# Kernel tuning notes

Measured on AMD Instinct MI355X. Metric: run time of the kernel, lower is better.

The kernel has to match this reference:

```python
import jax, jax.numpy as jnp
import numpy as np

EMBED = 1024
HEADS = 16
HDIM = EMBED // HEADS
B, S = 4, 2048
NEG = -1e20


def setup_inputs() -> dict:
    key = jax.random.key(0)
    ks = jax.random.split(key, 9)
    query = jax.random.normal(ks[0], (B, S, EMBED), dtype=jnp.float32)
    key_t = jax.random.normal(ks[1], (B, S, EMBED), dtype=jnp.float32)
    value = jax.random.normal(ks[2], (B, S, EMBED), dtype=jnp.float32)
    mask = jax.random.randint(ks[3], (1, 1, S, S), 0, 2, dtype=jnp.int32)
    padding = jax.random.randint(ks[4], (B, 1, 1, S), 0, 2, dtype=jnp.int32)
    sc = 1.0 / np.sqrt(EMBED)
    Wq = jax.random.normal(ks[5], (EMBED, EMBED), dtype=jnp.float32) * sc
    Wk = jax.random.normal(ks[6], (EMBED, EMBED), dtype=jnp.float32) * sc
    Wv = jax.random.normal(ks[7], (EMBED, EMBED), dtype=jnp.float32) * sc
    Wo = jax.random.normal(ks[8], (EMBED, EMBED), dtype=jnp.float32) * sc
    return {"query": query, "key": key_t, "value": value, "mask": mask,
            "padding": padding, "Wq": Wq, "Wk": Wk, "Wv": Wv, "Wo": Wo}


def reference(query, key, value, mask, padding, Wq, Wk, Wv, Wo):
    b, q_len, _ = query.shape
    k_len = key.shape[1]
    # projections (nn.Linear: x @ W^T), split into heads
    qs = (query @ Wq.T).reshape(b, q_len, HEADS, HDIM)
    ks = (key @ Wk.T).reshape(b, k_len, HEADS, HDIM)
    vs = (value @ Wv.T).reshape(b, k_len, HEADS, HDIM)
    scale = EMBED ** 0.25
    qs = qs / scale
    ks = ks / scale
    # [b, h, q, k] scores
    dot = jnp.einsum('bkhd,bqhd->bhqk', ks, qs)
    dot = jnp.where(mask == 0, NEG, dot)
    dot = jnp.where(padding == 0, NEG, dot)
    attn = jax.nn.softmax(dot, axis=-1)
    alpha = jnp.einsum('bhqk,bkhd->bqhd', attn, vs)
    out = alpha.reshape(b, q_len, EMBED) @ Wo.T
    return out
```

## Files before the change

kernel.cpp:

```cpp
#include <hip/hip_runtime.h>
#include <stdint.h>

#define B_  4
#define S_  2048
#define E_  1024
#define H_  16
#define D_  64

typedef __bf16 bf16;
typedef __bf16 bf16x4 __attribute__((ext_vector_type(4)));
typedef __bf16 bf16x8 __attribute__((ext_vector_type(8)));
typedef float  f32x4 __attribute__((ext_vector_type(4)));
typedef float  f32x16 __attribute__((ext_vector_type(16)));
typedef uint32_t u32x4 __attribute__((ext_vector_type(4)));

__device__ __forceinline__ f32x4 mfma16(bf16x8 a, bf16x8 b, f32x4 c) {
  return __builtin_amdgcn_mfma_f32_16x16x32_bf16(a, b, c, 0, 0, 0);
}
__device__ __forceinline__ f32x16 mfma32(bf16x8 a, bf16x8 b, f32x16 c) {
  return __builtin_amdgcn_mfma_f32_32x32x16_bf16(a, b, c, 0, 0, 0);
}

__device__ __forceinline__ int sw(int row, int idx) { return idx ^ ((row & 7) << 3); }

__device__ __forceinline__ void gl_lds16(const void* g, void* l) {
  __builtin_amdgcn_global_load_lds(
      (const __attribute__((address_space(1))) void*)g,
      (__attribute__((address_space(3))) void*)l, 16, 0, 0);
}

__device__ __forceinline__ uint32_t cvtpk(float lo, float hi) {
  uint32_t r;
  asm("v_cvt_pk_bf16_f32 %0, %1, %2" : "=v"(r) : "v"(lo), "v"(hi));
  return r;
}
__device__ __forceinline__ void plswap(uint32_t& a, uint32_t& b) {
  asm("v_permlane32_swap_b32 %0, %1" : "+v"(a), "+v"(b));
}

__global__ void pack_mask_kernel(const int* __restrict__ mask, uint32_t* __restrict__ mbits) {
  int idx = blockIdx.x * 256 + threadIdx.x;
  int q = idx >> 6, w = idx & 63;
  const int* p = mask + q * S_ + w * 32;
  uint32_t bits = 0;
#pragma unroll
  for (int j = 0; j < 32; j += 4) {
    int4 v = *(const int4*)(p + j);
    bits |= (v.x != 0 ? 1u : 0u) << (j + 0);
    bits |= (v.y != 0 ? 1u : 0u) << (j + 1);
    bits |= (v.z != 0 ? 1u : 0u) << (j + 2);
    bits |= (v.w != 0 ? 1u : 0u) << (j + 3);
  }
  mbits[idx] = bits;
}

__global__ void pack_pad_kernel(const int* __restrict__ pad, uint32_t* __restrict__ pbits) {
  int idx = threadIdx.x;
  int b = idx >> 6, w = idx & 63;
  const int* p = pad + b * S_ + w * 32;
  uint32_t bits = 0;
#pragma unroll
  for (int j = 0; j < 32; j += 4) {
    int4 v = *(const int4*)(p + j);
    bits |= (v.x != 0 ? 1u : 0u) << (j + 0);
    bits |= (v.y != 0 ? 1u : 0u) << (j + 1);
    bits |= (v.z != 0 ? 1u : 0u) << (j + 2);
    bits |= (v.w != 0 ? 1u : 0u) << (j + 3);
  }
  pbits[idx] = bits;
}

__global__ __launch_bounds__(256)
void cvt_act(const float* __restrict__ q, const float* __restrict__ k,
             const float* __restrict__ v, bf16* __restrict__ out) {
  const float* src = blockIdx.z == 0 ? q : (blockIdx.z == 1 ? k : v);
  size_t i = ((size_t)blockIdx.x * 256 + threadIdx.x) * 8;
  float4 a = *(const float4*)(src + i);
  float4 b = *(const float4*)(src + i + 4);
  bf16x8 o;
  o[0] = (bf16)a.x; o[1] = (bf16)a.y; o[2] = (bf16)a.z; o[3] = (bf16)a.w;
  o[4] = (bf16)b.x; o[5] = (bf16)b.y; o[6] = (bf16)b.z; o[7] = (bf16)b.w;
  *(bf16x8*)(out + (size_t)blockIdx.z * (8192ull * 1024ull) + i) = o;
}

__global__ __launch_bounds__(256)
void cvt_w(const float* __restrict__ w0, const float* __restrict__ w1,
           const float* __restrict__ w2, const float* __restrict__ w3,
           bf16* __restrict__ out, float sq, float sk) {
  int z = blockIdx.z;
  const float* src = z == 0 ? w0 : (z == 1 ? w1 : (z == 2 ? w2 : w3));
  float s = (z == 0) ? sq : ((z == 1) ? sk : 1.0f);
  size_t i = ((size_t)blockIdx.x * 256 + threadIdx.x) * 8;
  float4 a = *(const float4*)(src + i);
  float4 b = *(const float4*)(src + i + 4);
  bf16x8 o;
  o[0] = (bf16)(a.x * s); o[1] = (bf16)(a.y * s); o[2] = (bf16)(a.z * s); o[3] = (bf16)(a.w * s);
  o[4] = (bf16)(b.x * s); o[5] = (bf16)(b.y * s); o[6] = (bf16)(b.z * s); o[7] = (bf16)(b.w * s);
  *(bf16x8*)(out + (size_t)z * (1024ull * 1024ull) + i) = o;
}

struct GA { const bf16* A; const bf16* W; void* O; };

template<bool OUT_F32>
__global__ __launch_bounds__(256, 2)
void gemm_bf(GA g0, GA g1, GA g2) {
  GA g = (blockIdx.z == 0) ? g0 : ((blockIdx.z == 1) ? g1 : g2);
  const int tid = threadIdx.x;
  const int l = tid & 63, wv = tid >> 6;
  const int lg = l >> 4, lr = l & 15;
  const int wr = wv >> 1, wc = wv & 1;
  const int brow = blockIdx.x * 128, bcol = blockIdx.y * 128;
  const int sr = l >> 3, sc8 = l & 7;

  __shared__ bf16 Ls[2][128 * 64];
  bf16* As = Ls[0];
  bf16* Bs = Ls[1];

  f32x4 acc[4][4] = {};

  const bf16* Ab = g.A + (size_t)(brow + wv * 32 + sr) * E_ + (size_t)(sc8 ^ sr) * 8;
  const bf16* Bb = g.W + (size_t)(bcol + wv * 32 + sr) * E_ + (size_t)(sc8 ^ sr) * 8;
  bf16* la = As + (wv * 32) * 64;
  bf16* lb = Bs + (wv * 32) * 64;

  for (int kt = 0; kt < E_ / 64; ++kt) {
    __syncthreads();
    const bf16* a = Ab + kt * 64;
    const bf16* b = Bb + kt * 64;
#pragma unroll
    for (int i = 0; i < 4; ++i) {
      gl_lds16(a + (size_t)i * 8 * E_, la + i * 8 * 64);
      gl_lds16(b + (size_t)i * 8 * E_, lb + i * 8 * 64);
    }
    __syncthreads();
#pragma unroll
    for (int kk = 0; kk < 2; ++kk) {
      bf16x8 af[4], bfr[4];
#pragma unroll
      for (int ms = 0; ms < 4; ++ms) {
        int row = wr * 64 + ms * 16 + lr;
        af[ms] = *(const bf16x8*)&As[sw(row, row * 64 + kk * 32 + lg * 8)];
      }
#pragma unroll
      for (int ns = 0; ns < 4; ++ns) {
        int row = wc * 64 + ns * 16 + lr;
        bfr[ns] = *(const bf16x8*)&Bs[sw(row, row * 64 + kk * 32 + lg * 8)];
      }
#pragma unroll
      for (int ms = 0; ms < 4; ++ms)
#pragma unroll
        for (int ns = 0; ns < 4; ++ns)
          acc[ms][ns] = mfma16(af[ms], bfr[ns], acc[ms][ns]);
    }
  }

  if (!OUT_F32 && blockIdx.z == 2) {
    bf16* T = &Ls[0][0];
    __syncthreads();
#pragma unroll
    for (int ms = 0; ms < 4; ++ms) {
#pragma unroll
      for (int ns = 0; ns < 4; ++ns) {
        int col = wc * 64 + ns * 16 + lr;
        int rowb = wr * 64 + ms * 16 + lg * 4;
        bf16x4 hv;
#pragma unroll
        for (int r = 0; r < 4; ++r) hv[r] = (bf16)acc[ms][ns][r];
        *(bf16x4*)&T[col * 128 + (rowb ^ ((col & 7) << 3))] = hv;
      }
    }
    __syncthreads();
    int chunk = tid & 15, dl0 = tid >> 4;
#pragma unroll
    for (int pass = 0; pass < 8; ++pass) {
      int dl = pass * 16 + dl0;
      bf16x8 v = *(const bf16x8*)&T[dl * 128 + ((chunk * 8) ^ ((dl & 7) << 3))];
      int colg = bcol + dl;
      int bh2 = (brow >> 11) * 16 + (colg >> 6);
      int d = colg & 63;
      int s0 = (brow & 2047) + chunk * 8;
      *(bf16x8*)((bf16*)g.O + ((size_t)bh2 * 64 + d) * (size_t)S_ + s0) = v;
    }
    return;
  }

#pragma unroll
  for (int ms = 0; ms < 4; ++ms) {
#pragma unroll
    for (int ns = 0; ns < 4; ++ns) {
#pragma unroll
      for (int r = 0; r < 4; ++r) {
        int row = brow + wr * 64 + ms * 16 + lg * 4 + r;
        int col = bcol + wc * 64 + ns * 16 + lr;
        if constexpr (OUT_F32) ((float*)g.O)[(size_t)row * E_ + col] = acc[ms][ns][r];
        else                   ((bf16*)g.O)[(size_t)row * E_ + col] = (bf16)acc[ms][ns][r];
      }
    }
  }
}

__global__ __launch_bounds__(256, 4)
void attn_kernel(const bf16* __restrict__ Q, const bf16* __restrict__ K,
                 const bf16* __restrict__ Vt, const uint32_t* __restrict__ mbits,
                 const uint32_t* __restrict__ pbits, bf16* __restrict__ alpha) {
  const int raw = blockIdx.x;
  const int xcd = raw & 7, slot = raw >> 3;
  const int bh = xcd * 8 + (slot >> 4), qblk = slot & 15;
  const int b = bh >> 4, h = bh & 15;
  const int tid = threadIdx.x, wv = tid >> 6, l = tid & 63;
  const int ln = l & 31, hi = l >> 5;
  const int qw = qblk * 128 + wv * 32;
  const int sr = l >> 3, sc8 = l & 7;
  const int g = (ln & 7) ^ (ln >> 3);

  __shared__ bf16 Ks[2][64 * 64];
  __shared__ bf16 Vs[2][64 * 64];

  bf16x8 qreg[4];
#pragma unroll
  for (int dc = 0; dc < 4; ++dc)
    qreg[dc] = *(const bf16x8*)(Q + (size_t)(b * S_ + qw + ln) * E_ + h * 64 + dc * 16 + hi * 8);

  bf16x8 ones;
#pragma unroll
  for (int j = 0; j < 8; ++j) ones[j] = (bf16)1.0f;

  f32x16 o[2] = {};
  f32x16 lacc = {};

  const bf16* Kb = K + (size_t)b * S_ * E_ + (size_t)h * 64;
  const bf16* Vb = Vt + (size_t)bh * 64 * S_;

  auto stage = [&](int buf, int kt) {
#pragma unroll
    for (int op = 0; op < 2; ++op) {
      int rb = wv * 16 + op * 8;
      int cK = (sc8 ^ sr ^ ((rb >> 3) & 7)) * 8;
      gl_lds16(Kb + (size_t)(kt * 64 + rb + sr) * E_ + cK, Ks[buf] + rb * 64);
      gl_lds16(Vb + (size_t)(rb + sr) * S_ + kt * 64 + cK, Vs[buf] + rb * 64);
    }
  };

  stage(0, 0);
  __syncthreads();

  for (int kt = 0; kt < S_ / 64; ++kt) {
    const int cur = kt & 1;
    if (kt + 1 < S_ / 64) stage(cur ^ 1, kt + 1);

    f32x16 sc[2] = {};
    __builtin_amdgcn_s_setprio(1);
#pragma unroll
    for (int ct = 0; ct < 2; ++ct) {
#pragma unroll
      for (int dc = 0; dc < 4; ++dc) {
        int row = ct * 32 + ln;
        int c = (dc * 2 + hi) ^ g ^ (ct * 4);
        bf16x8 kf = *(const bf16x8*)&Ks[cur][row * 64 + c * 8];
        sc[ct] = mfma32(kf, qreg[dc], sc[ct]);
      }
    }
    __builtin_amdgcn_s_setprio(0);

    uint32_t pw0 = pbits[b * 64 + kt * 2], pw1 = pbits[b * 64 + kt * 2 + 1];
    uint2 mv = *(const uint2*)(mbits + (size_t)(qw + ln) * 64 + kt * 2);
    uint32_t mq[2];
    mq[0] = (mv.x & pw0) >> (hi * 4);
    mq[1] = (mv.y & pw1) >> (hi * 4);

    uint32_t up[16];
#pragma unroll
    for (int ct = 0; ct < 2; ++ct) {
      float p[16];
#pragma unroll
      for (int r = 0; r < 16; ++r) {
        const int rel = (r & 3) + 8 * (r >> 2);
        float pe = __builtin_amdgcn_exp2f(sc[ct][r]);
        uint32_t keep = (uint32_t)__builtin_amdgcn_sbfe(mq[ct], rel, 1);
        p[r] = __builtin_bit_cast(float, __builtin_bit_cast(uint32_t, pe) & keep);
      }
#pragma unroll
      for (int j = 0; j < 8; ++j)
        up[ct * 8 + j] = cvtpk(p[2 * j], p[2 * j + 1]);
    }

#pragma unroll
    for (int kc = 0; kc < 4; ++kc) {
      const int ct = kc >> 1, base = ct * 8 + (kc & 1) * 4;
      plswap(up[base + 0], up[base + 2]);
      plswap(up[base + 1], up[base + 3]);
      u32x4 w = {up[base + 0], up[base + 1], up[base + 2], up[base + 3]};
      bf16x8 pf = __builtin_bit_cast(bf16x8, w);
      __builtin_amdgcn_s_setprio(1);
#pragma unroll
      for (int dt = 0; dt < 2; ++dt) {
        int row = dt * 32 + ln;
        int c = (kc * 2 + hi) ^ g ^ (dt * 4);
        bf16x8 vf = *(const bf16x8*)&Vs[cur][row * 64 + c * 8];
        o[dt] = mfma32(vf, pf, o[dt]);
      }
      lacc = mfma32(ones, pf, lacc);
      __builtin_amdgcn_s_setprio(0);
    }
    __syncthreads();
  }

  float inv = 1.0f / lacc[0];
  size_t qoff = (size_t)(b * S_ + qw + ln) * E_ + h * 64;
#pragma unroll
  for (int dt = 0; dt < 2; ++dt) {
#pragma unroll
    for (int rg = 0; rg < 4; ++rg) {
      bf16x4 ov;
#pragma unroll
      for (int j = 0; j < 4; ++j) ov[j] = (bf16)(o[dt][rg * 4 + j] * inv);
      *(bf16x4*)(alpha + qoff + dt * 32 + rg * 8 + hi * 4) = ov;
    }
  }
}

extern "C" void kernel_launch(void* const* d_in, const int* in_sizes, int n_in,
                              void* d_out, int out_size, void* d_ws, size_t ws_size,
                              hipStream_t stream) {
  const float* query = (const float*)d_in[0];
  const float* key_t = (const float*)d_in[1];
  const float* value = (const float*)d_in[2];
  const int*   mask  = (const int*)d_in[3];
  const int*   pad   = (const int*)d_in[4];
  const float* Wq    = (const float*)d_in[5];
  const float* Wk    = (const float*)d_in[6];
  const float* Wv    = (const float*)d_in[7];
  const float* Wo    = (const float*)d_in[8];

  char* ws = (char*)d_ws;
  bf16* Abuf  = (bf16*)ws;
  bf16* alpha = (bf16*)(ws + ((size_t)16 << 20));
  bf16* Wb    = (bf16*)(ws + ((size_t)48 << 20));
  bf16* QKV   = (bf16*)(ws + ((size_t)56 << 20));
  uint32_t* mbits = (uint32_t*)(ws + ((size_t)104 << 20));
  uint32_t* pbits = mbits + (size_t)S_ * 64;

  const size_t AM = 8192ull * 1024ull;
  const size_t WM = 1024ull * 1024ull;
  bf16* Vt = QKV + 2 * AM;

  pack_mask_kernel<<<512, 256, 0, stream>>>(mask, mbits);
  pack_pad_kernel<<<1, 256, 0, stream>>>(pad, pbits);

  cvt_act<<<dim3(4096, 1, 3), 256, 0, stream>>>(query, key_t, value, Abuf);
  const float qscale = 0.17677669529663687f;
  const float log2e  = 1.4426950408889634f;
  cvt_w<<<dim3(512, 1, 4), 256, 0, stream>>>(Wq, Wk, Wv, Wo, Wb, qscale * log2e, qscale);

  GA gq{Abuf,          Wb,          QKV};
  GA gk{Abuf + AM,     Wb + WM,     QKV + AM};
  GA gv{Abuf + 2 * AM, Wb + 2 * WM, Vt};
  gemm_bf<false><<<dim3(64, 8, 3), 256, 0, stream>>>(gq, gk, gv);

  attn_kernel<<<1024, 256, 0, stream>>>(QKV, QKV + AM, Vt, mbits, pbits, alpha);

  GA go{alpha, Wb + 3 * WM, d_out};
  gemm_bf<true><<<dim3(64, 8, 1), 256, 0, stream>>>(go, go, go);
}
```

Measured before the change: 222.9 us.

## Precombine mask with padding into transposed layout and remap GEMM block order

Adds a small kernel that ANDs the packed causal mask with the padding bits per batch and stores them transposed [b][kt][q], so the attention inner loop does one coalesced uint2 load instead of a strided row load plus two padding loads. The GEMM grid becomes 1D with an XCD-aware swizzle of block rows/cols, and launch bounds are raised to 4 waves per SIMD target. This adds an extra launch and 2 MB of mask traffic, and the occupancy hint may cause register spills in the GEMM.

Measured after the change: 222.6 us. About the same (-0.2%).

```diff
diff --git a/kernel.cpp b/kernel.cpp
--- a/kernel.cpp
+++ b/kernel.cpp
@@ -68,6 +68,19 @@
     bits |= (v.w != 0 ? 1u : 0u) << (j + 3);
   }
   pbits[idx] = bits;
+}
+
+__global__ __launch_bounds__(256)
+void expand_mask(const uint32_t* __restrict__ mbits, const uint32_t* __restrict__ pbits,
+                 uint2* __restrict__ mbt) {
+  int idx = blockIdx.x * 256 + threadIdx.x;
+  int q = idx & 2047;
+  int kt = (idx >> 11) & 31;
+  int b = idx >> 16;
+  uint2 r;
+  r.x = mbits[q * 64 + kt * 2 + 0] & pbits[b * 64 + kt * 2 + 0];
+  r.y = mbits[q * 64 + kt * 2 + 1] & pbits[b * 64 + kt * 2 + 1];
+  mbt[idx] = r;
 }
 
 __global__ __launch_bounds__(256)
@@ -102,14 +115,16 @@
 struct GA { const bf16* A; const bf16* W; void* O; };
 
 template<bool OUT_F32>
-__global__ __launch_bounds__(256, 2)
+__global__ __launch_bounds__(256, 4)
 void gemm_bf(GA g0, GA g1, GA g2) {
   GA g = (blockIdx.z == 0) ? g0 : ((blockIdx.z == 1) ? g1 : g2);
+  const int id = blockIdx.x;
+  const int brow = ((id & 7) * 8 + (id >> 6)) * 128;
+  const int bcol = ((id >> 3) & 7) * 128;
   const int tid = threadIdx.x;
   const int l = tid & 63, wv = tid >> 6;
   const int lg = l >> 4, lr = l & 15;
   const int wr = wv >> 1, wc = wv & 1;
-  const int brow = blockIdx.x * 128, bcol = blockIdx.y * 128;
   const int sr = l >> 3, sc8 = l & 7;
 
   __shared__ bf16 Ls[2][128 * 64];
@@ -201,8 +216,8 @@
 
 __global__ __launch_bounds__(256, 4)
 void attn_kernel(const bf16* __restrict__ Q, const bf16* __restrict__ K,
-                 const bf16* __restrict__ Vt, const uint32_t* __restrict__ mbits,
-                 const uint32_t* __restrict__ pbits, bf16* __restrict__ alpha) {
+                 const bf16* __restrict__ Vt, const uint2* __restrict__ mbt,
+                 bf16* __restrict__ alpha) {
   const int raw = blockIdx.x;
   const int xcd = raw & 7, slot = raw >> 3;
   const int bh = xcd * 8 + (slot >> 4), qblk = slot & 15;
@@ -230,6 +245,7 @@
 
   const bf16* Kb = K + (size_t)b * S_ * E_ + (size_t)h * 64;
   const bf16* Vb = Vt + (size_t)bh * 64 * S_;
+  const uint2* mrow = mbt + ((size_t)b << 16) + qw + ln;
 
   auto stage = [&](int buf, int kt) {
 #pragma unroll
@@ -262,11 +278,10 @@
     }
     __builtin_amdgcn_s_setprio(0);
 
-    uint32_t pw0 = pbits[b * 64 + kt * 2], pw1 = pbits[b * 64 + kt * 2 + 1];
-    uint2 mv = *(const uint2*)(mbits + (size_t)(qw + ln) * 64 + kt * 2);
+    uint2 mv = mrow[kt << 11];
     uint32_t mq[2];
-    mq[0] = (mv.x & pw0) >> (hi * 4);
-    mq[1] = (mv.y & pw1) >> (hi * 4);
+    mq[0] = mv.x >> (hi * 4);
+    mq[1] = mv.y >> (hi * 4);
 
     uint32_t up[16];
 #pragma unroll
@@ -339,6 +354,7 @@
   bf16* QKV   = (bf16*)(ws + ((size_t)56 << 20));
   uint32_t* mbits = (uint32_t*)(ws + ((size_t)104 << 20));
   uint32_t* pbits = mbits + (size_t)S_ * 64;
+  uint2*    mbt   = (uint2*)(ws + ((size_t)105 << 20));
 
   const size_t AM = 8192ull * 1024ull;
   const size_t WM = 1024ull * 1024ull;
@@ -346,6 +362,7 @@
 
   pack_mask_kernel<<<512, 256, 0, stream>>>(mask, mbits);
   pack_pad_kernel<<<1, 256, 0, stream>>>(pad, pbits);
+  expand_mask<<<1024, 256, 0, stream>>>(mbits, pbits, mbt);
 
   cvt_act<<<dim3(4096, 1, 3), 256, 0, stream>>>(query, key_t, value, Abuf);
   const float qscale = 0.17677669529663687f;
@@ -355,10 +372,10 @@
   GA gq{Abuf,          Wb,          QKV};
   GA gk{Abuf + AM,     Wb + WM,     QKV + AM};
   GA gv{Abuf + 2 * AM, Wb + 2 * WM, Vt};
-  gemm_bf<false><<<dim3(64, 8, 3), 256, 0, stream>>>(gq, gk, gv);
-
-  attn_kernel<<<1024, 256, 0, stream>>>(QKV, QKV + AM, Vt, mbits, pbits, alpha);
+  gemm_bf<false><<<dim3(512, 1, 3), 256, 0, stream>>>(gq, gk, gv);
+
+  attn_kernel<<<1024, 256, 0, stream>>>(QKV, QKV + AM, Vt, mbt, alpha);
 
   GA go{alpha, Wb + 3 * WM, d_out};
-  gemm_bf<true><<<dim3(64, 8, 1), 256, 0, stream>>>(go, go, go);
-}
+  gemm_bf<true><<<dim3(512, 1, 1), 256, 0, stream>>>(go, go, go);
+}
```
